# Performance work log

Measured on AMD Instinct MI355X. Metric: run time of the kernel, lower is better.

## Reference

```python
import jax, jax.numpy as jnp
import numpy as np
import math

B, C, T = 8, 512, 4096
CHUNK = 16          # AR_CHUNK_TOK
H = 8               # heads
DH = C // H
CODE_DIM = 96
N_BOOKS = 8
N_EMBED = 1024
EPS = 1e-5
NCH = T // CHUNK


def _posenc(c, t):
    pos = np.arange(t)[:, None].astype(np.float64)
    div = np.exp(np.arange(0, c, 2) * (-math.log(10000.0) / c))
    pe = np.zeros((t, c), np.float32)
    pe[:, 0::2] = np.sin(pos * div)
    pe[:, 1::2] = np.cos(pos * div)
    return jnp.asarray(pe.T)  # [C, t]


def _ln(x, g, b):
    m = x.mean(-1, keepdims=True)
    v = ((x - m) ** 2).mean(-1, keepdims=True)
    return (x - m) * jax.lax.rsqrt(v + EPS) * g + b


def setup_inputs() -> dict:
    ks = jax.random.split(jax.random.key(0), 16)
    w = lambda i, s: jax.random.normal(ks[i], s, jnp.float32) * 0.02
    return dict(
        qa=jax.random.normal(ks[0], (B, C, T), jnp.float32),
        zt=jax.random.normal(ks[1], (B, C, T), jnp.float32),
        lnq_g=jnp.ones((C,), jnp.float32), lnq_b=jnp.zeros((C,), jnp.float32),
        lnkv_g=jnp.ones((C,), jnp.float32), lnkv_b=jnp.zeros((C,), jnp.float32),
        Wq=w(2, (C, C)), Wk=w(3, (C, C)), Wv=w(4, (C, C)), Wo=w(5, (C, C)),
        ffn_g=jnp.ones((C,), jnp.float32), ffn_b=jnp.zeros((C,), jnp.float32),
        W1=w(6, (C, 2 * C)), b1=jnp.zeros((2 * C,), jnp.float32),
        W2=w(7, (2 * C, C)), b2=jnp.zeros((C,), jnp.float32),
        tn_g=jnp.ones((C,), jnp.float32), tn_b=jnp.zeros((C,), jnp.float32),
        scale=jnp.float32(0.08),
        Wd=w(8, (CODE_DIM, C)), bd=jnp.zeros((CODE_DIM,), jnp.float32),
        Wu=w(9, (C, CODE_DIM)), bu=jnp.zeros((C,), jnp.float32),
        books=jax.random.normal(ks[10], (N_BOOKS, N_EMBED, CODE_DIM), jnp.float32) / math.sqrt(CODE_DIM),
    )


def _forward(qa, zt, lnq_g, lnq_b, lnkv_g, lnkv_b, Wq, Wk, Wv, Wo, ffn_g, ffn_b,
             W1, b1, W2, b2, tn_g, tn_b, scale, Wd, bd, Wu, bu, books):
    pe = _posenc(C, CHUNK)  # [C, 16], chunk-local positions as in the torch loop
    qa_c = qa.reshape(B, C, NCH, CHUNK).transpose(2, 0, 1, 3)  # [NCH, B, C, 16]
    zt_c = zt.reshape(B, C, NCH, CHUNK).transpose(2, 0, 1, 3)
    sc = jnp.clip(scale, 0.005, 0.5)

    def split(x):  # [B,16,C] -> [B,H,16,DH]
        return x.reshape(B, CHUNK, H, DH).transpose(0, 2, 1, 3)

    def step(prev_last, xs):
        # zt_prev is [prev chunk's last z_hat token, zeros...]: z_run is zero-initialized
        # and only positions < s are written when chunk s reads it.
        qa_k, zt_k = xs
        zt_prev = jnp.concatenate(
            [prev_last[:, :, None], jnp.zeros((B, C, CHUNK - 1), qa_k.dtype)], axis=-1)
        # CrossPredictor (dropout is identity in eval)
        q = _ln((zt_prev + pe).transpose(0, 2, 1), lnq_g, lnq_b)   # [B,16,C]
        kv = _ln((qa_k + pe).transpose(0, 2, 1), lnkv_g, lnkv_b)   # [B,16,C]
        Q, K, V = split(q @ Wq), split(kv @ Wk), split(kv @ Wv)
        attn = jax.nn.softmax(jnp.einsum('bhqd,bhkd->bhqk', Q, K) / math.sqrt(DH), axis=-1)
        ctx = jnp.einsum('bhqk,bhkd->bhqd', attn, V).transpose(0, 2, 1, 3).reshape(B, CHUNK, C)
        y = ctx @ Wo + q
        y = y + jax.nn.gelu(_ln(y, ffn_g, ffn_b) @ W1 + b1, approximate=False) @ W2 + b2
        z_pred = y.transpose(0, 2, 1)  # [B,C,16]
        # residual -> tanh(TokenNorm) -> scale -> 1x1 conv down
        r = zt_k - jax.lax.stop_gradient(z_pred)
        rN = jnp.tanh(_ln(r.transpose(0, 2, 1), tn_g, tn_b)).transpose(0, 2, 1)
        rD = jnp.einsum('dc,bct->bdt', Wd, sc * rN) + bd[:, None]  # [B,96,16]
        # residual VQ over N_BOOKS codebooks (straight-through)
        x = rD.transpose(0, 2, 1).reshape(B * CHUNK, CODE_DIM)
        residual = x
        q_sum = jnp.zeros_like(x)
        for k in range(N_BOOKS):
            emb = jax.lax.stop_gradient(books[k])
            idx = jnp.argmax(residual @ emb.T - 0.5 * jnp.sum(emb * emb, axis=1), axis=1)
            qv = emb[idx]
            q_sum = q_sum + jax.lax.stop_gradient(qv - residual) + residual
            residual = residual - qv
        qD = q_sum.reshape(B, CHUNK, CODE_DIM).transpose(0, 2, 1)  # [B,96,16]
        z_hat = jnp.einsum('cd,bdt->bct', Wu, qD) + bu[:, None] + z_pred
        return z_hat[:, :, -1], z_hat

    _, ys = jax.lax.scan(step, jnp.zeros((B, C), qa.dtype), (qa_c, zt_c))
    return ys.transpose(1, 2, 0, 3).reshape(B, C, T)  # z_run [B,C,T]


def reference(qa, zt, lnq_g, lnq_b, lnkv_g, lnkv_b, Wq, Wk, Wv, Wo, ffn_g, ffn_b,
              W1, b1, W2, b2, tn_g, tn_b, scale, Wd, bd, Wu, bu, books):
    return _forward(qa, zt, lnq_g, lnq_b, lnkv_g, lnkv_b, Wq, Wk, Wv, Wo, ffn_g, ffn_b,
                    W1, b1, W2, b2, tn_g, tn_b, scale, Wd, bd, Wu, bu, books)
```

## Files before the change

kernel.cpp:

```cpp
#include <hip/hip_runtime.h>
#include <math.h>

#define Bsz 8
#define Cdim 512
#define Tdim 4096
#define NHq 8
#define CD 96
#define NB 8
#define NE 1024
#define NCHq 256
#define Mtok (Bsz*Tdim)
#define M2tok (Bsz*NCHq)

typedef __attribute__((ext_vector_type(8))) short bf16x8;
typedef __attribute__((ext_vector_type(4))) float f32x4;
typedef unsigned int uint;
typedef unsigned short ushort;

__global__ __launch_bounds__(256) void pe_qc_kernel(float* pe_tab, float* qc_ln,
        const float* __restrict__ lnq_g, const float* __restrict__ lnq_b){
  int t = blockIdx.x;
  int tid = threadIdx.x;
  __shared__ float red[256];
  double f = -log(10000.0) / (double)Cdim;
  float v[2];
  #pragma unroll
  for (int u = 0; u < 2; ++u){
    int c = tid + u*256;
    int ce = c & ~1;
    double ang = (double)t * exp(f * (double)ce);
    v[u] = (float)((c & 1) ? cos(ang) : sin(ang));
    pe_tab[t*Cdim + c] = v[u];
  }
  red[tid] = v[0] + v[1]; __syncthreads();
  for (int s = 128; s > 0; s >>= 1){ if (tid < s) red[tid] += red[tid+s]; __syncthreads(); }
  float mean = red[0] * (1.f/512.f); __syncthreads();
  float d0 = v[0]-mean, d1 = v[1]-mean;
  red[tid] = d0*d0 + d1*d1; __syncthreads();
  for (int s = 128; s > 0; s >>= 1){ if (tid < s) red[tid] += red[tid+s]; __syncthreads(); }
  float rstd = 1.0f/sqrtf(red[0]*(1.f/512.f) + 1e-5f);
  qc_ln[t*Cdim + tid]       = d0*rstd*lnq_g[tid]     + lnq_b[tid];
  qc_ln[t*Cdim + tid + 256] = d1*rstd*lnq_g[tid+256] + lnq_b[tid+256];
}

__global__ __launch_bounds__(256) void ln_rows_kernel(const float* __restrict__ src, float* __restrict__ dst,
        const float* __restrict__ g, const float* __restrict__ bia, int mode, const float* __restrict__ scale_ptr){
  int row = blockIdx.x; int tid = threadIdx.x;
  const float* sr = src + (size_t)row*Cdim;
  float v0 = sr[tid], v1 = sr[tid+256];
  __shared__ float red[256];
  red[tid] = v0+v1; __syncthreads();
  for (int s = 128; s > 0; s >>= 1){ if (tid < s) red[tid] += red[tid+s]; __syncthreads(); }
  float mean = red[0]*(1.f/512.f); __syncthreads();
  float d0 = v0-mean, d1 = v1-mean;
  red[tid] = d0*d0 + d1*d1; __syncthreads();
  for (int s = 128; s > 0; s >>= 1){ if (tid < s) red[tid] += red[tid+s]; __syncthreads(); }
  float rstd = 1.0f/sqrtf(red[0]*(1.f/512.f) + 1e-5f);
  float h0 = d0*rstd*g[tid]     + bia[tid];
  float h1 = d1*rstd*g[tid+256] + bia[tid+256];
  if (mode == 1){
    float sc = *scale_ptr; sc = fminf(fmaxf(sc, 0.005f), 0.5f);
    h0 = tanhf(h0)*sc; h1 = tanhf(h1)*sc;
  }
  float* dr = dst + (size_t)row*Cdim;
  dr[tid] = h0; dr[tid+256] = h1;
}

__global__ void tin_kernel(const float* __restrict__ qa, const float* __restrict__ pe_tab, float* __restrict__ rows){
  __shared__ float tile[32][33];
  int b = blockIdx.z, c0 = blockIdx.y*32, t0 = blockIdx.x*32;
  int tx = threadIdx.x, ty = threadIdx.y;
  int t = t0 + tx;
  #pragma unroll
  for (int j = 0; j < 4; j++){
    int c = c0 + ty + j*8;
    tile[ty+j*8][tx] = qa[((size_t)(b*Cdim + c))*Tdim + t] + pe_tab[(t & 15)*Cdim + c];
  }
  __syncthreads();
  #pragma unroll
  for (int j = 0; j < 4; j++){
    int tt = t0 + ty + j*8;
    rows[((size_t)(b*Tdim + tt))*Cdim + c0 + tx] = tile[tx][ty+j*8];
  }
}

__global__ void resid_kernel(const float* __restrict__ zt, const float* __restrict__ zp_rows, float* __restrict__ rows){
  __shared__ float tile[32][33];
  int b = blockIdx.z, c0 = blockIdx.y*32, t0 = blockIdx.x*32;
  int tx = threadIdx.x, ty = threadIdx.y;
  int t = t0 + tx;
  #pragma unroll
  for (int j = 0; j < 4; j++){
    int c = c0 + ty + j*8;
    tile[ty+j*8][tx] = zt[((size_t)(b*Cdim + c))*Tdim + t];
  }
  __syncthreads();
  #pragma unroll
  for (int j = 0; j < 4; j++){
    int tt = t0 + ty + j*8;
    size_t o = ((size_t)(b*Tdim + tt))*Cdim + c0 + tx;
    rows[o] = tile[tx][ty+j*8] - zp_rows[o];
  }
}

__global__ void tout_kernel(const float* __restrict__ rows, float* __restrict__ out){
  __shared__ float tile[32][33];
  int b = blockIdx.z, c0 = blockIdx.y*32, t0 = blockIdx.x*32;
  int tx = threadIdx.x, ty = threadIdx.y;
  #pragma unroll
  for (int j = 0; j < 4; j++){
    int tt = t0 + ty + j*8;
    tile[ty+j*8][tx] = rows[((size_t)(b*Tdim + tt))*Cdim + c0 + tx];
  }
  __syncthreads();
  #pragma unroll
  for (int j = 0; j < 4; j++){
    int c = c0 + ty + j*8;
    out[((size_t)(b*Cdim + c))*Tdim + t0 + tx] = tile[tx][ty+j*8];
  }
}

__global__ void twd_kernel(const float* __restrict__ Wd, float* __restrict__ WdT){
  int i = blockIdx.x*256 + threadIdx.x; if (i >= 96*512) return;
  int kq = i / 96, n = i % 96;
  WdT[i] = Wd[(size_t)n*512 + kq];
}

__global__ void tbt_kernel(const float* __restrict__ books, float* __restrict__ booksT){
  __shared__ float tile[32][33];
  int k = blockIdx.z, d0 = blockIdx.y*32, c0 = blockIdx.x*32;
  int tx = threadIdx.x, ty = threadIdx.y;
  #pragma unroll
  for (int j = 0; j < 4; j++){
    int c = c0 + ty + j*8;
    tile[ty+j*8][tx] = books[((size_t)k*NE + c)*CD + d0 + tx];
  }
  __syncthreads();
  #pragma unroll
  for (int j = 0; j < 4; j++){
    int d = d0 + ty + j*8;
    booksT[(size_t)k*CD*NE + (size_t)d*NE + c0 + tx] = tile[tx][ty+j*8];
  }
}

__global__ void hb_kernel(const float* __restrict__ books, float* __restrict__ hb){
  int j = blockIdx.x*256 + threadIdx.x;
  if (j >= NB*NE) return;
  const float* e = books + (size_t)j*CD;
  float s = 0.f;
  #pragma unroll
  for (int d = 0; d < CD; d++) s = fmaf(e[d], e[d], s);
  hb[j] = 0.5f*s;
}

__device__ __forceinline__ uint pack_hi(float a, float b){
  uint ua = __float_as_uint(a), ub = __float_as_uint(b);
  return (ua >> 16) | (ub & 0xFFFF0000u);
}
__device__ __forceinline__ uint pack_lo(float a, float b){
  float ha = __uint_as_float(__float_as_uint(a) & 0xFFFF0000u);
  float hb = __uint_as_float(__float_as_uint(b) & 0xFFFF0000u);
  return pack_hi(a - ha, b - hb);
}

__global__ void cvtT_kernel(const float* __restrict__ W, ushort* __restrict__ hT, ushort* __restrict__ lT,
        int K, int N){
  __shared__ float tile[32][33];
  int k0 = blockIdx.y*32, n0 = blockIdx.x*32;
  int tx = threadIdx.x, ty = threadIdx.y;
  #pragma unroll
  for (int j = 0; j < 4; j++)
    tile[ty+j*8][tx] = W[(size_t)(k0+ty+j*8)*N + n0+tx];
  __syncthreads();
  #pragma unroll
  for (int j = 0; j < 4; j++){
    int n = n0 + ty + j*8;
    float f = tile[tx][ty+j*8];
    uint u = __float_as_uint(f);
    float hf = __uint_as_float(u & 0xFFFF0000u);
    hT[(size_t)n*K + k0 + tx] = (ushort)(u >> 16);
    lT[(size_t)n*K + k0 + tx] = (ushort)(__float_as_uint(f - hf) >> 16);
  }
}

__global__ void cvtP_kernel(const float* __restrict__ X, ushort* __restrict__ h, ushort* __restrict__ lo, int n){
  int i = blockIdx.x*256 + threadIdx.x; if (i >= n) return;
  float f = X[i];
  uint u = __float_as_uint(f);
  float hf = __uint_as_float(u & 0xFFFF0000u);
  h[i]  = (ushort)(u >> 16);
  lo[i] = (ushort)(__float_as_uint(f - hf) >> 16);
}

__global__ __launch_bounds__(256) void gemm_kernel(const float* __restrict__ A, const float* __restrict__ Bm,
        float* __restrict__ Cm, int M, int N, int K,
        const float* __restrict__ bias, const float* __restrict__ addbuf, int addmode, int act){
  __shared__ float As[16][65];
  __shared__ float Bs[16][64];
  int l = threadIdx.x;
  int tx = l & 15, ty = l >> 4;
  int m0 = blockIdx.y*64, n0 = blockIdx.x*64;
  int ai = l >> 2, ak = (l & 3)*4;
  int bk = l >> 4, bj = (l & 15)*4;
  float acc[4][4] = {{0.f}};
  bool nfull = (n0 + 64 <= N);
  for (int k0 = 0; k0 < K; k0 += 16){
    float4 av = make_float4(0.f, 0.f, 0.f, 0.f);
    if (m0 + ai < M) av = *(const float4*)(A + (size_t)(m0+ai)*K + k0 + ak);
    As[ak][ai] = av.x; As[ak+1][ai] = av.y; As[ak+2][ai] = av.z; As[ak+3][ai] = av.w;
    if (nfull){
      *(float4*)(&Bs[bk][bj]) = *(const float4*)(Bm + (size_t)(k0+bk)*N + n0 + bj);
    } else {
      #pragma unroll
      for (int u = 0; u < 4; u++){
        int n = n0 + bj + u;
        Bs[bk][bj+u] = (n < N) ? Bm[(size_t)(k0+bk)*N + n] : 0.f;
      }
    }
    __syncthreads();
    #pragma unroll
    for (int kk = 0; kk < 16; kk++){
      float a0 = As[kk][ty*4], a1 = As[kk][ty*4+1], a2 = As[kk][ty*4+2], a3 = As[kk][ty*4+3];
      float b0 = Bs[kk][tx*4], b1 = Bs[kk][tx*4+1], b2 = Bs[kk][tx*4+2], b3 = Bs[kk][tx*4+3];
      acc[0][0] = fmaf(a0,b0,acc[0][0]); acc[0][1] = fmaf(a0,b1,acc[0][1]);
      acc[0][2] = fmaf(a0,b2,acc[0][2]); acc[0][3] = fmaf(a0,b3,acc[0][3]);
      acc[1][0] = fmaf(a1,b0,acc[1][0]); acc[1][1] = fmaf(a1,b1,acc[1][1]);
      acc[1][2] = fmaf(a1,b2,acc[1][2]); acc[1][3] = fmaf(a1,b3,acc[1][3]);
      acc[2][0] = fmaf(a2,b0,acc[2][0]); acc[2][1] = fmaf(a2,b1,acc[2][1]);
      acc[2][2] = fmaf(a2,b2,acc[2][2]); acc[2][3] = fmaf(a2,b3,acc[2][3]);
      acc[3][0] = fmaf(a3,b0,acc[3][0]); acc[3][1] = fmaf(a3,b1,acc[3][1]);
      acc[3][2] = fmaf(a3,b2,acc[3][2]); acc[3][3] = fmaf(a3,b3,acc[3][3]);
    }
    __syncthreads();
  }
  #pragma unroll
  for (int r = 0; r < 4; r++){
    int m = m0 + ty*4 + r; if (m >= M) continue;
    #pragma unroll
    for (int c = 0; c < 4; c++){
      int n = n0 + tx*4 + c; if (n >= N) continue;
      float v = acc[r][c];
      if (bias) v += bias[n];
      if (act == 1) v = 0.5f*v*(1.0f + erff(v*0.7071067811865475f));
      if (addmode == 1) v += addbuf[(size_t)(m & 15)*N + n];
      else if (addmode == 2) v += addbuf[(size_t)m*N + n];
      Cm[(size_t)m*N + n] = v;
    }
  }
}

__global__ __launch_bounds__(256, 1) void mgemm_kernel(const float* __restrict__ A,
        const ushort* __restrict__ BhT, const ushort* __restrict__ BlT,
        float* __restrict__ Cm, int M, int N, int K,
        const float* __restrict__ bias, const float* __restrict__ addbuf, int addmode, int act){
  __shared__ __align__(16) ushort Ah[128][32];
  __shared__ __align__(16) ushort Al[128][32];
  __shared__ __align__(16) ushort Bh[128][32];
  __shared__ __align__(16) ushort Bl[128][32];
  int l = threadIdx.x;
  int il = l & 63, wv = l >> 6;
  int wr = wv >> 1, wc = wv & 1;
  int fr = il & 15, fg = il >> 4;
  int m0 = blockIdx.y*128, n0 = blockIdx.x*128;
  int srow = l >> 1, shalf = (l & 1) * 16;
  const float*  Ap  = A   + (size_t)(m0 + srow)*K + shalf;
  const ushort* Bhp = BhT + (size_t)(n0 + srow)*K + shalf;
  const ushort* Blp = BlT + (size_t)(n0 + srow)*K + shalf;
  f32x4 acc[4][4];
  #pragma unroll
  for (int i = 0; i < 4; i++)
    #pragma unroll
    for (int j = 0; j < 4; j++)
      acc[i][j] = (f32x4){0.f, 0.f, 0.f, 0.f};
  for (int k0 = 0; k0 < K; k0 += 32){
    float4 a0 = *(const float4*)(Ap + k0);
    float4 a1 = *(const float4*)(Ap + k0 + 4);
    float4 a2 = *(const float4*)(Ap + k0 + 8);
    float4 a3 = *(const float4*)(Ap + k0 + 12);
    uint4 bh0 = *(const uint4*)(Bhp + k0);
    uint4 bh1 = *(const uint4*)(Bhp + k0 + 8);
    uint4 bl0 = *(const uint4*)(Blp + k0);
    uint4 bl1 = *(const uint4*)(Blp + k0 + 8);
    __syncthreads();
    uint4 h0, h1, l0v, l1v;
    h0.x = pack_hi(a0.x,a0.y); h0.y = pack_hi(a0.z,a0.w);
    h0.z = pack_hi(a1.x,a1.y); h0.w = pack_hi(a1.z,a1.w);
    h1.x = pack_hi(a2.x,a2.y); h1.y = pack_hi(a2.z,a2.w);
    h1.z = pack_hi(a3.x,a3.y); h1.w = pack_hi(a3.z,a3.w);
    l0v.x = pack_lo(a0.x,a0.y); l0v.y = pack_lo(a0.z,a0.w);
    l0v.z = pack_lo(a1.x,a1.y); l0v.w = pack_lo(a1.z,a1.w);
    l1v.x = pack_lo(a2.x,a2.y); l1v.y = pack_lo(a2.z,a2.w);
    l1v.z = pack_lo(a3.x,a3.y); l1v.w = pack_lo(a3.z,a3.w);
    *(uint4*)&Ah[srow][shalf]   = h0;  *(uint4*)&Ah[srow][shalf+8] = h1;
    *(uint4*)&Al[srow][shalf]   = l0v; *(uint4*)&Al[srow][shalf+8] = l1v;
    *(uint4*)&Bh[srow][shalf]   = bh0; *(uint4*)&Bh[srow][shalf+8] = bh1;
    *(uint4*)&Bl[srow][shalf]   = bl0; *(uint4*)&Bl[srow][shalf+8] = bl1;
    __syncthreads();
    bf16x8 afh[4], afl[4], bfh[4], bfl[4];
    #pragma unroll
    for (int q = 0; q < 4; q++){
      afh[q] = *(const bf16x8*)&Ah[wr*64 + q*16 + fr][fg*8];
      afl[q] = *(const bf16x8*)&Al[wr*64 + q*16 + fr][fg*8];
      bfh[q] = *(const bf16x8*)&Bh[wc*64 + q*16 + fr][fg*8];
      bfl[q] = *(const bf16x8*)&Bl[wc*64 + q*16 + fr][fg*8];
    }
    #pragma unroll
    for (int i = 0; i < 4; i++)
      #pragma unroll
      for (int j = 0; j < 4; j++)
        acc[i][j] = __builtin_amdgcn_mfma_f32_16x16x32_bf16(afh[i], bfh[j], acc[i][j], 0, 0, 0);
    #pragma unroll
    for (int i = 0; i < 4; i++)
      #pragma unroll
      for (int j = 0; j < 4; j++)
        acc[i][j] = __builtin_amdgcn_mfma_f32_16x16x32_bf16(afh[i], bfl[j], acc[i][j], 0, 0, 0);
    #pragma unroll
    for (int i = 0; i < 4; i++)
      #pragma unroll
      for (int j = 0; j < 4; j++)
        acc[i][j] = __builtin_amdgcn_mfma_f32_16x16x32_bf16(afl[i], bfh[j], acc[i][j], 0, 0, 0);
  }
  #pragma unroll
  for (int i = 0; i < 4; i++){
    #pragma unroll
    for (int j = 0; j < 4; j++){
      #pragma unroll
      for (int r = 0; r < 4; r++){
        int m = m0 + wr*64 + i*16 + fg*4 + r;
        int n = n0 + wc*64 + j*16 + fr;
        float v = acc[i][j][r];
        if (bias) v += bias[n];
        if (act == 1) v = 0.5f*v*(1.0f + erff(v*0.7071067811865475f));
        if (addmode == 1) v += addbuf[(size_t)(m & 15)*N + n];
        else if (addmode == 2) v += addbuf[(size_t)m*N + n];
        Cm[(size_t)m*N + n] = v;
      }
    }
  }
}

__global__ __launch_bounds__(128) void attn1_kernel(const float* __restrict__ Kb, const float* __restrict__ Vb,
        const float* __restrict__ Qp, float* __restrict__ ctxb){
  int idx = blockIdx.x;
  int b = idx >> 8, ch = idx & 255;
  size_t m0 = (size_t)b*Tdim + ch*16;
  int t = threadIdx.x >> 3, h = threadIdx.x & 7;
  const float* q = Qp + t*Cdim + h*64;
  float qr[64];
  #pragma unroll
  for (int d = 0; d < 64; d += 4){ float4 f = *(const float4*)(q+d); qr[d]=f.x; qr[d+1]=f.y; qr[d+2]=f.z; qr[d+3]=f.w; }
  float s[16];
  #pragma unroll
  for (int k = 0; k < 16; k++){
    const float* kr = Kb + (m0+k)*Cdim + h*64;
    float acc = 0.f;
    #pragma unroll
    for (int d = 0; d < 64; d += 4){
      float4 f = *(const float4*)(kr+d);
      acc = fmaf(qr[d],f.x,acc); acc = fmaf(qr[d+1],f.y,acc);
      acc = fmaf(qr[d+2],f.z,acc); acc = fmaf(qr[d+3],f.w,acc);
    }
    s[k] = acc * 0.125f;
  }
  float mx = s[0];
  #pragma unroll
  for (int k = 1; k < 16; k++) mx = fmaxf(mx, s[k]);
  float sum = 0.f;
  #pragma unroll
  for (int k = 0; k < 16; k++){ s[k] = expf(s[k]-mx); sum += s[k]; }
  float inv = 1.0f/sum;
  float ctx[64];
  #pragma unroll
  for (int d = 0; d < 64; d++) ctx[d] = 0.f;
  #pragma unroll
  for (int k = 0; k < 16; k++){
    float p = s[k]*inv;
    const float* vr = Vb + (m0+k)*Cdim + h*64;
    #pragma unroll
    for (int d = 0; d < 64; d += 4){
      float4 f = *(const float4*)(vr+d);
      ctx[d]=fmaf(p,f.x,ctx[d]); ctx[d+1]=fmaf(p,f.y,ctx[d+1]);
      ctx[d+2]=fmaf(p,f.z,ctx[d+2]); ctx[d+3]=fmaf(p,f.w,ctx[d+3]);
    }
  }
  float* o = ctxb + (m0+t)*Cdim + h*64;
  #pragma unroll
  for (int d = 0; d < 64; d += 4){
    float4 f; f.x=ctx[d]; f.y=ctx[d+1]; f.z=ctx[d+2]; f.w=ctx[d+3];
    *(float4*)(o+d) = f;
  }
}

__global__ __launch_bounds__(64) void attn2_kernel(const float* __restrict__ Kb, const float* __restrict__ Vb,
        const float* __restrict__ Qp, float* __restrict__ ctxb){
  int m2 = blockIdx.x;
  int b = m2 >> 8, ch = m2 & 255;
  size_t m0 = (size_t)b*Tdim + ch*16;
  int h = threadIdx.x;
  if (h >= 8) return;
  const float* q = Qp + (size_t)m2*Cdim + h*64;
  float qr[64];
  #pragma unroll
  for (int d = 0; d < 64; d += 4){ float4 f = *(const float4*)(q+d); qr[d]=f.x; qr[d+1]=f.y; qr[d+2]=f.z; qr[d+3]=f.w; }
  float s[16];
  #pragma unroll
  for (int k = 0; k < 16; k++){
    const float* kr = Kb + (m0+k)*Cdim + h*64;
    float acc = 0.f;
    #pragma unroll
    for (int d = 0; d < 64; d += 4){
      float4 f = *(const float4*)(kr+d);
      acc = fmaf(qr[d],f.x,acc); acc = fmaf(qr[d+1],f.y,acc);
      acc = fmaf(qr[d+2],f.z,acc); acc = fmaf(qr[d+3],f.w,acc);
    }
    s[k] = acc * 0.125f;
  }
  float mx = s[0];
  #pragma unroll
  for (int k = 1; k < 16; k++) mx = fmaxf(mx, s[k]);
  float sum = 0.f;
  #pragma unroll
  for (int k = 0; k < 16; k++){ s[k] = expf(s[k]-mx); sum += s[k]; }
  float inv = 1.0f/sum;
  float ctx[64];
  #pragma unroll
  for (int d = 0; d < 64; d++) ctx[d] = 0.f;
  #pragma unroll
  for (int k = 0; k < 16; k++){
    float p = s[k]*inv;
    const float* vr = Vb + (m0+k)*Cdim + h*64;
    #pragma unroll
    for (int d = 0; d < 64; d += 4){
      float4 f = *(const float4*)(vr+d);
      ctx[d]=fmaf(p,f.x,ctx[d]); ctx[d+1]=fmaf(p,f.y,ctx[d+1]);
      ctx[d+2]=fmaf(p,f.z,ctx[d+2]); ctx[d+3]=fmaf(p,f.w,ctx[d+3]);
    }
  }
  float* o = ctxb + (size_t)m2*Cdim + h*64;
  #pragma unroll
  for (int d = 0; d < 64; d += 4){
    float4 f; f.x=ctx[d]; f.y=ctx[d+1]; f.z=ctx[d+2]; f.w=ctx[d+3];
    *(float4*)(o+d) = f;
  }
}

__global__ __launch_bounds__(256) void q2_kernel(const float* __restrict__ dout, float* __restrict__ p2q,
        const float* __restrict__ g, const float* __restrict__ bia){
  int m2 = blockIdx.x; int tid = threadIdx.x;
  int b = m2 >> 8, ch = m2 & 255;
  int tprev = ch*16 - 1;
  float v0, v1;
  {
    int c = tid;
    float carry = (ch == 0) ? 0.f : dout[((size_t)(b*Cdim + c))*Tdim + tprev];
    v0 = carry + ((c & 1) ? 1.f : 0.f);
  }
  {
    int c = tid + 256;
    float carry = (ch == 0) ? 0.f : dout[((size_t)(b*Cdim + c))*Tdim + tprev];
    v1 = carry + ((c & 1) ? 1.f : 0.f);
  }
  __shared__ float red[256];
  red[tid] = v0+v1; __syncthreads();
  for (int s = 128; s > 0; s >>= 1){ if (tid < s) red[tid] += red[tid+s]; __syncthreads(); }
  float mean = red[0]*(1.f/512.f); __syncthreads();
  float d0 = v0-mean, d1 = v1-mean;
  red[tid] = d0*d0 + d1*d1; __syncthreads();
  for (int s = 128; s > 0; s >>= 1){ if (tid < s) red[tid] += red[tid+s]; __syncthreads(); }
  float rstd = 1.0f/sqrtf(red[0]*(1.f/512.f) + 1e-5f);
  p2q[(size_t)m2*Cdim + tid]       = d0*rstd*g[tid]     + bia[tid];
  p2q[(size_t)m2*Cdim + tid + 256] = d1*rstd*g[tid+256] + bia[tid+256];
}

__global__ __launch_bounds__(256) void r2_kernel(const float* __restrict__ zt, const float* __restrict__ zp,
        float* __restrict__ out){
  int m2 = blockIdx.x; int tid = threadIdx.x;
  int b = m2 >> 8, ch = m2 & 255; int t0 = ch*16;
  #pragma unroll
  for (int u = 0; u < 2; u++){
    int c = tid + u*256;
    out[(size_t)m2*Cdim + c] = zt[((size_t)(b*Cdim + c))*Tdim + t0] - zp[(size_t)m2*Cdim + c];
  }
}

__global__ __launch_bounds__(256) void scatter2_kernel(const float* __restrict__ z, float* __restrict__ dout){
  int m2 = blockIdx.x; int tid = threadIdx.x;
  int b = m2 >> 8, ch = m2 & 255; int t0 = ch*16;
  #pragma unroll
  for (int u = 0; u < 2; u++){
    int c = tid + u*256;
    dout[((size_t)(b*Cdim + c))*Tdim + t0] = z[(size_t)m2*Cdim + c];
  }
}

template<int MT>
__global__ __launch_bounds__(256, 1) void vqg_kernel(float* __restrict__ x,
        const float* __restrict__ books, const float* __restrict__ booksT,
        const float* __restrict__ hb){
  constexpr int MI  = MT/16;
  constexpr int TPT = 256/MT;
  constexpr int F4  = 24/TPT;
  int l = threadIdx.x;
  int tx = l & 15, ty = l >> 4;
  int tok = l / TPT, part = l % TPT;
  size_t tok0 = (size_t)blockIdx.x * MT;
  __shared__ float As[96][MT];
  __shared__ float Es[96][128];
  __shared__ float hs[128];
  __shared__ float sb[MT][16];
  __shared__ int   si[MT][16];
  __shared__ int   sel[MT];
  float* xp = x + (tok0 + tok)*CD;
  #pragma unroll
  for (int j = 0; j < F4; j++){
    int d4 = part*F4 + j;
    float4 v = *(const float4*)(xp + d4*4);
    As[d4*4+0][tok]=v.x; As[d4*4+1][tok]=v.y; As[d4*4+2][tok]=v.z; As[d4*4+3][tok]=v.w;
  }
  for (int k = 0; k < NB; k++){
    const float* bT = booksT + (size_t)k*CD*NE;
    float best[MI]; int bidx[MI];
    #pragma unroll
    for (int i = 0; i < MI; i++){ best[i] = -3.0e38f; bidx[i] = 0; }
    for (int t = 0; t < 8; t++){
      int n0 = t*128;
      __syncthreads();
      #pragma unroll
      for (int j = 0; j < 12; j++){
        int f4 = j*256 + l;
        int d = f4 >> 5, c4 = f4 & 31;
        float4 v = *(const float4*)(bT + (size_t)d*NE + n0 + c4*4);
        *(float4*)(&Es[d][c4*4]) = v;
      }
      if (l < 32){
        float4 hv = *(const float4*)(hb + k*NE + n0 + l*4);
        *(float4*)(&hs[l*4]) = hv;
      }
      __syncthreads();
      float acc[MI][8];
      #pragma unroll
      for (int i = 0; i < MI; i++)
        #pragma unroll
        for (int j = 0; j < 8; j++) acc[i][j] = 0.f;
      #pragma unroll 2
      for (int kk = 0; kk < 96; kk++){
        float av[MI], bw[8];
        #pragma unroll
        for (int g = 0; g < MI/4; g++)
          *(float4*)(av + g*4) = *(const float4*)(&As[kk][g*64 + ty*4]);
        *(float4*)(bw)   = *(const float4*)(&Es[kk][tx*4]);
        *(float4*)(bw+4) = *(const float4*)(&Es[kk][64 + tx*4]);
        #pragma unroll
        for (int i = 0; i < MI; i++)
          #pragma unroll
          for (int j = 0; j < 8; j++)
            acc[i][j] = fmaf(av[i], bw[j], acc[i][j]);
      }
      #pragma unroll
      for (int i = 0; i < MI; i++){
        #pragma unroll
        for (int j = 0; j < 8; j++){
          int cl = (j>>2)*64 + tx*4 + (j&3);
          float s = acc[i][j] - hs[cl];
          if (s > best[i]){ best[i] = s; bidx[i] = n0 + cl; }
        }
      }
    }
    #pragma unroll
    for (int i = 0; i < MI; i++){
      int row = (i>>2)*64 + ty*4 + (i&3);
      sb[row][tx] = best[i]; si[row][tx] = bidx[i];
    }
    __syncthreads();
    if (l < MT){
      float bb = sb[l][0]; int bi = si[l][0];
      #pragma unroll
      for (int t2 = 1; t2 < 16; t2++){
        float b2 = sb[l][t2]; int i2 = si[l][t2];
        if (b2 > bb || (b2 == bb && i2 < bi)){ bb = b2; bi = i2; }
      }
      sel[l] = bi;
    }
    __syncthreads();
    int s = sel[tok];
    const float* e = books + ((size_t)k*NE + s)*CD;
    #pragma unroll
    for (int j = 0; j < F4; j++){
      int d4 = part*F4 + j;
      float4 v = *(const float4*)(e + d4*4);
      As[d4*4+0][tok] -= v.x; As[d4*4+1][tok] -= v.y;
      As[d4*4+2][tok] -= v.z; As[d4*4+3][tok] -= v.w;
    }
  }
  #pragma unroll
  for (int j = 0; j < F4; j++){
    int d4 = part*F4 + j;
    float4 xo = *(const float4*)(xp + d4*4);
    float4 q;
    q.x = xo.x - As[d4*4+0][tok];
    q.y = xo.y - As[d4*4+1][tok];
    q.z = xo.z - As[d4*4+2][tok];
    q.w = xo.w - As[d4*4+3][tok];
    *(float4*)(xp + d4*4) = q;
  }
}

extern "C" void kernel_launch(void* const* d_in, const int* in_sizes, int n_in,
                              void* d_out, int out_size, void* d_ws, size_t ws_size,
                              hipStream_t stream) {
  const float* qa    = (const float*)d_in[0];
  const float* zt    = (const float*)d_in[1];
  const float* lnq_g = (const float*)d_in[2];
  const float* lnq_b = (const float*)d_in[3];
  const float* lnkv_g= (const float*)d_in[4];
  const float* lnkv_b= (const float*)d_in[5];
  const float* Wq    = (const float*)d_in[6];
  const float* Wk    = (const float*)d_in[7];
  const float* Wv    = (const float*)d_in[8];
  const float* Wo    = (const float*)d_in[9];
  const float* ffn_g = (const float*)d_in[10];
  const float* ffn_b = (const float*)d_in[11];
  const float* W1    = (const float*)d_in[12];
  const float* b1    = (const float*)d_in[13];
  const float* W2    = (const float*)d_in[14];
  const float* b2    = (const float*)d_in[15];
  const float* tn_g  = (const float*)d_in[16];
  const float* tn_b  = (const float*)d_in[17];
  const float* scale = (const float*)d_in[18];
  const float* Wd    = (const float*)d_in[19];
  const float* bd    = (const float*)d_in[20];
  const float* Wu    = (const float*)d_in[21];
  const float* bu    = (const float*)d_in[22];
  const float* books = (const float*)d_in[23];
  float* out = (float*)d_out;

  float* ws = (float*)d_ws;
  size_t off = 0;
  float* pe_tab  = ws + off; off += 16*512;
  float* qc_ln   = ws + off; off += 16*512;
  float* qc_proj = ws + off; off += 16*512;
  float* WdT     = ws + off; off += 512*96;
  float* hbuf    = ws + off; off += 8*1024;
  ushort* wub = (ushort*)(ws + off); off += 2146304;
  ushort* WqTh = wub;            ushort* WqTl = WqTh + 262144;
  ushort* WkTh = WqTl + 262144;  ushort* WkTl = WkTh + 262144;
  ushort* WvTh = WkTl + 262144;  ushort* WvTl = WvTh + 262144;
  ushort* WoTh = WvTl + 262144;  ushort* WoTl = WoTh + 262144;
  ushort* W1Th = WoTl + 262144;  ushort* W1Tl = W1Th + 524288;
  ushort* W2Th = W1Tl + 524288;  ushort* W2Tl = W2Th + 524288;
  ushort* WuPh = W2Tl + 524288;  ushort* WuPl = WuPh + 49152;
  float* bA      = ws + off; off += (size_t)Mtok*512;
  float* bK      = ws + off; off += (size_t)Mtok*512;
  float* bV      = ws + off; off += (size_t)Mtok*512;
  float* bH      = ws + off; off += (size_t)4096*1024;
  float* bX      = bH;
  float* booksTp = bH + (size_t)Mtok*CD;
  float* bY      = out;

  float* p2q   = bA;
  float* p2Qp  = bA + 1048576;
  float* p2ctx = bA + 2*1048576;
  float* p2y   = bA + 3*1048576;
  float* p2lny = bA + 4*1048576;
  float* p2h   = bA + 5*1048576;
  float* p2r   = bA + 7*1048576;
  float* p2x   = bA + 8*1048576;
  float* p2z   = bA + 8*1048576 + 196608;

  dim3 tpb32(32, 8);
  dim3 tgrid(Tdim/32, Cdim/32, Bsz);

  hipLaunchKernelGGL(pe_qc_kernel, dim3(16), dim3(256), 0, stream, pe_tab, qc_ln, lnq_g, lnq_b);
  hipLaunchKernelGGL(twd_kernel, dim3((96*512+255)/256), dim3(256), 0, stream, Wd, WdT);
  hipLaunchKernelGGL(hb_kernel, dim3((NB*NE+255)/256), dim3(256), 0, stream, books, hbuf);
  hipLaunchKernelGGL(cvtT_kernel, dim3(16, 16), tpb32, 0, stream, Wq, WqTh, WqTl, 512, 512);
  hipLaunchKernelGGL(cvtT_kernel, dim3(16, 16), tpb32, 0, stream, Wk, WkTh, WkTl, 512, 512);
  hipLaunchKernelGGL(cvtT_kernel, dim3(16, 16), tpb32, 0, stream, Wv, WvTh, WvTl, 512, 512);
  hipLaunchKernelGGL(cvtT_kernel, dim3(16, 16), tpb32, 0, stream, Wo, WoTh, WoTl, 512, 512);
  hipLaunchKernelGGL(cvtT_kernel, dim3(32, 16), tpb32, 0, stream, W1, W1Th, W1Tl, 512, 1024);
  hipLaunchKernelGGL(cvtT_kernel, dim3(16, 32), tpb32, 0, stream, W2, W2Th, W2Tl, 1024, 512);
  hipLaunchKernelGGL(cvtP_kernel, dim3((512*96+255)/256), dim3(256), 0, stream, Wu, WuPh, WuPl, 512*96);

  hipLaunchKernelGGL(tin_kernel, tgrid, tpb32, 0, stream, qa, pe_tab, bA);
  hipLaunchKernelGGL(ln_rows_kernel, dim3(Mtok), dim3(256), 0, stream, bA, bA, lnkv_g, lnkv_b, 0, scale);
  hipLaunchKernelGGL(mgemm_kernel, dim3(4, Mtok/128), dim3(256), 0, stream, bA, WkTh, WkTl, bK, Mtok, 512, 512,
                     (const float*)nullptr, (const float*)nullptr, 0, 0);
  hipLaunchKernelGGL(mgemm_kernel, dim3(4, Mtok/128), dim3(256), 0, stream, bA, WvTh, WvTl, bV, Mtok, 512, 512,
                     (const float*)nullptr, (const float*)nullptr, 0, 0);
  hipLaunchKernelGGL(gemm_kernel, dim3(8, 1), dim3(256), 0, stream, qc_ln, Wq, qc_proj, 16, 512, 512,
                     (const float*)nullptr, (const float*)nullptr, 0, 0);

  hipLaunchKernelGGL(attn1_kernel, dim3(M2tok), dim3(128), 0, stream, bK, bV, qc_proj, bA);
  hipLaunchKernelGGL(mgemm_kernel, dim3(4, Mtok/128), dim3(256), 0, stream, bA, WoTh, WoTl, bY, Mtok, 512, 512,
                     (const float*)nullptr, qc_ln, 1, 0);
  hipLaunchKernelGGL(ln_rows_kernel, dim3(Mtok), dim3(256), 0, stream, bY, bA, ffn_g, ffn_b, 0, scale);
  for (int p = 0; p < 8; p++){
    size_t mo = (size_t)p*4096;
    hipLaunchKernelGGL(mgemm_kernel, dim3(8, 4096/128), dim3(256), 0, stream, bA + mo*512, W1Th, W1Tl, bH, 4096, 1024, 512,
                       b1, (const float*)nullptr, 0, 1);
    hipLaunchKernelGGL(mgemm_kernel, dim3(4, 4096/128), dim3(256), 0, stream, bH, W2Th, W2Tl, bY + mo*512, 4096, 512, 1024,
                       b2, bY + mo*512, 2, 0);
  }

  hipLaunchKernelGGL(resid_kernel, tgrid, tpb32, 0, stream, zt, bY, bA);
  hipLaunchKernelGGL(ln_rows_kernel, dim3(Mtok), dim3(256), 0, stream, bA, bA, tn_g, tn_b, 1, scale);
  hipLaunchKernelGGL(gemm_kernel, dim3(2, Mtok/64), dim3(256), 0, stream, bA, WdT, bX, Mtok, 96, 512,
                     bd, (const float*)nullptr, 0, 0);
  hipLaunchKernelGGL(tbt_kernel, dim3(NE/32, CD/32, NB), tpb32, 0, stream, books, booksTp);
  hipLaunchKernelGGL(vqg_kernel<128>, dim3(Mtok/128), dim3(256), 0, stream, bX, books, booksTp, hbuf);
  hipLaunchKernelGGL(mgemm_kernel, dim3(4, Mtok/128), dim3(256), 0, stream, bX, WuPh, WuPl, bA, Mtok, 512, 96,
                     bu, bY, 2, 0);
  hipLaunchKernelGGL(tout_kernel, tgrid, tpb32, 0, stream, bA, out);

  hipLaunchKernelGGL(q2_kernel, dim3(M2tok), dim3(256), 0, stream, out, p2q, lnq_g, lnq_b);
  hipLaunchKernelGGL(mgemm_kernel, dim3(4, M2tok/128), dim3(256), 0, stream, p2q, WqTh, WqTl, p2Qp, M2tok, 512, 512,
                     (const float*)nullptr, (const float*)nullptr, 0, 0);
  hipLaunchKernelGGL(attn2_kernel, dim3(M2tok), dim3(64), 0, stream, bK, bV, p2Qp, p2ctx);
  hipLaunchKernelGGL(mgemm_kernel, dim3(4, M2tok/128), dim3(256), 0, stream, p2ctx, WoTh, WoTl, p2y, M2tok, 512, 512,
                     (const float*)nullptr, p2q, 2, 0);
  hipLaunchKernelGGL(ln_rows_kernel, dim3(M2tok), dim3(256), 0, stream, p2y, p2lny, ffn_g, ffn_b, 0, scale);
  hipLaunchKernelGGL(mgemm_kernel, dim3(8, M2tok/128), dim3(256), 0, stream, p2lny, W1Th, W1Tl, p2h, M2tok, 1024, 512,
                     b1, (const float*)nullptr, 0, 1);
  hipLaunchKernelGGL(mgemm_kernel, dim3(4, M2tok/128), dim3(256), 0, stream, p2h, W2Th, W2Tl, p2y, M2tok, 512, 1024,
                     b2, p2y, 2, 0);
  hipLaunchKernelGGL(r2_kernel, dim3(M2tok), dim3(256), 0, stream, zt, p2y, p2r);
  hipLaunchKernelGGL(ln_rows_kernel, dim3(M2tok), dim3(256), 0, stream, p2r, p2r, tn_g, tn_b, 1, scale);
  hipLaunchKernelGGL(gemm_kernel, dim3(2, M2tok/64), dim3(256), 0, stream, p2r, WdT, p2x, M2tok, 96, 512,
                     bd, (const float*)nullptr, 0, 0);
  hipLaunchKernelGGL(vqg_kernel<64>, dim3(M2tok/64), dim3(256), 0, stream, p2x, books, booksTp, hbuf);
  hipLaunchKernelGGL(mgemm_kernel, dim3(4, M2tok/128), dim3(256), 0, stream, p2x, WuPh, WuPl, p2z, M2tok, 512, 96,
                     bu, p2y, 2, 0);
  hipLaunchKernelGGL(scatter2_kernel, dim3(M2tok), dim3(256), 0, stream, p2z, out);

  (void)in_sizes; (void)n_in; (void)out_size; (void)ws_size;
}
```

Baseline: 3.733 ms.

## Widen VQ codebook tile and split small-batch VQ across codebook chunks

The large-batch VQ kernel now uses a 128x256 register tile (8x16 per thread) with 256-code chunks and a shuffle-based argmax instead of a shared-memory reduction. The small second-pass VQ, which only had 32 blocks, is split into per-codebook launches: one kernel computes partial argmaxes over 8 code chunks in parallel, and a second merges them and updates the residual. This aims to raise arithmetic intensity in the big pass and to fill the GPU in the small pass. The cost is more registers and LDS in vq1, and 16 extra launches plus workspace round-trips in the second pass.

```diff
diff --git a/kernel.cpp b/kernel.cpp
--- a/kernel.cpp
+++ b/kernel.cpp
@@ -493,73 +493,68 @@
   }
 }
 
-template<int MT>
-__global__ __launch_bounds__(256, 1) void vqg_kernel(float* __restrict__ x,
+__global__ __launch_bounds__(256, 1) void vq1_kernel(float* __restrict__ x,
         const float* __restrict__ books, const float* __restrict__ booksT,
         const float* __restrict__ hb){
-  constexpr int MI  = MT/16;
-  constexpr int TPT = 256/MT;
-  constexpr int F4  = 24/TPT;
   int l = threadIdx.x;
   int tx = l & 15, ty = l >> 4;
-  int tok = l / TPT, part = l % TPT;
-  size_t tok0 = (size_t)blockIdx.x * MT;
-  __shared__ float As[96][MT];
-  __shared__ float Es[96][128];
-  __shared__ float hs[128];
-  __shared__ float sb[MT][16];
-  __shared__ int   si[MT][16];
-  __shared__ int   sel[MT];
+  int tok = l >> 1, part = l & 1;
+  size_t tok0 = (size_t)blockIdx.x * 128;
+  __shared__ float As[96][128];
+  __shared__ float Es[96][256];
+  __shared__ float hs[256];
+  __shared__ int   sel[128];
   float* xp = x + (tok0 + tok)*CD;
   #pragma unroll
-  for (int j = 0; j < F4; j++){
-    int d4 = part*F4 + j;
+  for (int j = 0; j < 12; j++){
+    int d4 = part*12 + j;
     float4 v = *(const float4*)(xp + d4*4);
     As[d4*4+0][tok]=v.x; As[d4*4+1][tok]=v.y; As[d4*4+2][tok]=v.z; As[d4*4+3][tok]=v.w;
   }
   for (int k = 0; k < NB; k++){
     const float* bT = booksT + (size_t)k*CD*NE;
-    float best[MI]; int bidx[MI];
-    #pragma unroll
-    for (int i = 0; i < MI; i++){ best[i] = -3.0e38f; bidx[i] = 0; }
-    for (int t = 0; t < 8; t++){
-      int n0 = t*128;
+    const float* hk = hb + k*NE;
+    float best[8]; int bidx[8];
+    #pragma unroll
+    for (int i = 0; i < 8; i++){ best[i] = -3.0e38f; bidx[i] = 0; }
+    for (int t = 0; t < 4; t++){
+      int n0 = t*256;
       __syncthreads();
       #pragma unroll
-      for (int j = 0; j < 12; j++){
+      for (int j = 0; j < 24; j++){
         int f4 = j*256 + l;
-        int d = f4 >> 5, c4 = f4 & 31;
+        int d = f4 >> 6, c4 = f4 & 63;
         float4 v = *(const float4*)(bT + (size_t)d*NE + n0 + c4*4);
         *(float4*)(&Es[d][c4*4]) = v;
       }
-      if (l < 32){
-        float4 hv = *(const float4*)(hb + k*NE + n0 + l*4);
+      if (l < 64){
+        float4 hv = *(const float4*)(hk + n0 + l*4);
         *(float4*)(&hs[l*4]) = hv;
       }
       __syncthreads();
-      float acc[MI][8];
-      #pragma unroll
-      for (int i = 0; i < MI; i++)
+      float acc[8][16];
+      #pragma unroll
+      for (int i = 0; i < 8; i++)
         #pragma unroll
-        for (int j = 0; j < 8; j++) acc[i][j] = 0.f;
+        for (int j = 0; j < 16; j++) acc[i][j] = 0.f;
       #pragma unroll 2
       for (int kk = 0; kk < 96; kk++){
-        float av[MI], bw[8];
+        float av[8], bw[16];
+        *(float4*)(av)   = *(const float4*)(&As[kk][ty*8]);
+        *(float4*)(av+4) = *(const float4*)(&As[kk][ty*8+4]);
         #pragma unroll
-        for (int g = 0; g < MI/4; g++)
-          *(float4*)(av + g*4) = *(const float4*)(&As[kk][g*64 + ty*4]);
-        *(float4*)(bw)   = *(const float4*)(&Es[kk][tx*4]);
-        *(float4*)(bw+4) = *(const float4*)(&Es[kk][64 + tx*4]);
+        for (int p = 0; p < 4; p++)
+          *(float4*)(bw + p*4) = *(const float4*)(&Es[kk][p*64 + tx*4]);
         #pragma unroll
-        for (int i = 0; i < MI; i++)
+        for (int i = 0; i < 8; i++)
           #pragma unroll
-          for (int j = 0; j < 8; j++)
+          for (int j = 0; j < 16; j++)
             acc[i][j] = fmaf(av[i], bw[j], acc[i][j]);
       }
       #pragma unroll
-      for (int i = 0; i < MI; i++){
+      for (int i = 0; i < 8; i++){
         #pragma unroll
-        for (int j = 0; j < 8; j++){
+        for (int j = 0; j < 16; j++){
           int cl = (j>>2)*64 + tx*4 + (j&3);
           float s = acc[i][j] - hs[cl];
           if (s > best[i]){ best[i] = s; bidx[i] = n0 + cl; }
@@ -567,34 +562,30 @@
       }
     }
     #pragma unroll
-    for (int i = 0; i < MI; i++){
-      int row = (i>>2)*64 + ty*4 + (i&3);
-      sb[row][tx] = best[i]; si[row][tx] = bidx[i];
-    }
-    __syncthreads();
-    if (l < MT){
-      float bb = sb[l][0]; int bi = si[l][0];
-      #pragma unroll
-      for (int t2 = 1; t2 < 16; t2++){
-        float b2 = sb[l][t2]; int i2 = si[l][t2];
-        if (b2 > bb || (b2 == bb && i2 < bi)){ bb = b2; bi = i2; }
+    for (int i = 0; i < 8; i++){
+      float s = best[i]; int idx = bidx[i];
+      #pragma unroll
+      for (int m = 1; m < 16; m <<= 1){
+        float os = __shfl_xor(s, m);
+        int   oi = __shfl_xor(idx, m);
+        if (os > s || (os == s && oi < idx)){ s = os; idx = oi; }
       }
-      sel[l] = bi;
+      if (tx == 0) sel[ty*8 + i] = idx;
     }
     __syncthreads();
     int s = sel[tok];
     const float* e = books + ((size_t)k*NE + s)*CD;
     #pragma unroll
-    for (int j = 0; j < F4; j++){
-      int d4 = part*F4 + j;
+    for (int j = 0; j < 12; j++){
+      int d4 = part*12 + j;
       float4 v = *(const float4*)(e + d4*4);
       As[d4*4+0][tok] -= v.x; As[d4*4+1][tok] -= v.y;
       As[d4*4+2][tok] -= v.z; As[d4*4+3][tok] -= v.w;
     }
   }
   #pragma unroll
-  for (int j = 0; j < F4; j++){
-    int d4 = part*F4 + j;
+  for (int j = 0; j < 12; j++){
+    int d4 = part*12 + j;
     float4 xo = *(const float4*)(xp + d4*4);
     float4 q;
     q.x = xo.x - As[d4*4+0][tok];
@@ -602,6 +593,118 @@
     q.z = xo.z - As[d4*4+2][tok];
     q.w = xo.w - As[d4*4+3][tok];
     *(float4*)(xp + d4*4) = q;
+  }
+}
+
+__global__ __launch_bounds__(256, 2) void vq2a_kernel(const float* __restrict__ src,
+        const float* __restrict__ booksT, const float* __restrict__ hb,
+        float* __restrict__ ps, int* __restrict__ pi, int k){
+  int l = threadIdx.x;
+  int tx = l & 15, ty = l >> 4;
+  int cb = blockIdx.x;
+  int tok0 = blockIdx.y * 64;
+  int n0 = cb * 128;
+  __shared__ float As[96][64];
+  __shared__ float Es[96][128];
+  __shared__ float hs[128];
+  {
+    int tok = l >> 2, part = l & 3;
+    const float* sp = src + (size_t)(tok0 + tok)*CD;
+    #pragma unroll
+    for (int j = 0; j < 6; j++){
+      int d4 = part*6 + j;
+      float4 v = *(const float4*)(sp + d4*4);
+      As[d4*4+0][tok]=v.x; As[d4*4+1][tok]=v.y; As[d4*4+2][tok]=v.z; As[d4*4+3][tok]=v.w;
+    }
+  }
+  const float* bT = booksT + (size_t)k*CD*NE;
+  #pragma unroll
+  for (int j = 0; j < 12; j++){
+    int f4 = j*256 + l;
+    int d = f4 >> 5, c4 = f4 & 31;
+    float4 v = *(const float4*)(bT + (size_t)d*NE + n0 + c4*4);
+    *(float4*)(&Es[d][c4*4]) = v;
+  }
+  if (l < 32){
+    float4 hv = *(const float4*)(hb + k*NE + n0 + l*4);
+    *(float4*)(&hs[l*4]) = hv;
+  }
+  __syncthreads();
+  float acc[4][8];
+  #pragma unroll
+  for (int i = 0; i < 4; i++)
+    #pragma unroll
+    for (int j = 0; j < 8; j++) acc[i][j] = 0.f;
+  #pragma unroll 2
+  for (int kk = 0; kk < 96; kk++){
+    float av[4], bw[8];
+    *(float4*)(av)   = *(const float4*)(&As[kk][ty*4]);
+    *(float4*)(bw)   = *(const float4*)(&Es[kk][tx*4]);
+    *(float4*)(bw+4) = *(const float4*)(&Es[kk][64 + tx*4]);
+    #pragma unroll
+    for (int i = 0; i < 4; i++)
+      #pragma unroll
+      for (int j = 0; j < 8; j++)
+        acc[i][j] = fmaf(av[i], bw[j], acc[i][j]);
+  }
+  #pragma unroll
+  for (int i = 0; i < 4; i++){
+    float best = -3.0e38f; int bidx = 0;
+    #pragma unroll
+    for (int j = 0; j < 8; j++){
+      int cl = (j>>2)*64 + tx*4 + (j&3);
+      float s = acc[i][j] - hs[cl];
+      if (s > best){ best = s; bidx = n0 + cl; }
+    }
+    #pragma unroll
+    for (int m = 1; m < 16; m <<= 1){
+      float os = __shfl_xor(best, m);
+      int   oi = __shfl_xor(bidx, m);
+      if (os > best || (os == best && oi < bidx)){ best = os; bidx = oi; }
+    }
+    if (tx == 0){
+      int row = tok0 + ty*4 + i;
+      ps[cb*M2tok + row] = best;
+      pi[cb*M2tok + row] = bidx;
+    }
+  }
+}
+
+__global__ __launch_bounds__(256) void vq2b_kernel(float* __restrict__ x, float* __restrict__ res,
+        const float* __restrict__ books, const float* __restrict__ ps, const int* __restrict__ pi, int k){
+  int l = threadIdx.x;
+  int tok = blockIdx.x*32 + (l >> 3);
+  int part = l & 7;
+  float bb = ps[tok]; int bi = pi[tok];
+  #pragma unroll
+  for (int c = 1; c < 8; c++){
+    float s2 = ps[c*M2tok + tok]; int i2 = pi[c*M2tok + tok];
+    if (s2 > bb || (s2 == bb && i2 < bi)){ bb = s2; bi = i2; }
+  }
+  const float* e = books + ((size_t)k*NE + bi)*CD + part*12;
+  const float* sp = ((k == 0) ? (const float*)x : (const float*)res) + (size_t)tok*CD + part*12;
+  float r[12];
+  #pragma unroll
+  for (int j = 0; j < 12; j += 4){
+    float4 sv = *(const float4*)(sp + j);
+    float4 ev = *(const float4*)(e + j);
+    r[j]=sv.x-ev.x; r[j+1]=sv.y-ev.y; r[j+2]=sv.z-ev.z; r[j+3]=sv.w-ev.w;
+  }
+  if (k < NB-1){
+    float* rp = res + (size_t)tok*CD + part*12;
+    #pragma unroll
+    for (int j = 0; j < 12; j += 4){
+      float4 v; v.x=r[j]; v.y=r[j+1]; v.z=r[j+2]; v.w=r[j+3];
+      *(float4*)(rp + j) = v;
+    }
+  } else {
+    float* xq = x + (size_t)tok*CD + part*12;
+    #pragma unroll
+    for (int j = 0; j < 12; j += 4){
+      float4 xo = *(const float4*)(xq + j);
+      float4 v; v.x=xo.x-r[j]; v.y=xo.y-r[j+1]; v.z=xo.z-r[j+2]; v.w=xo.w-r[j+3];
+      *(float4*)(xq + j) = v;
+    }
   }
 }
 
@@ -666,6 +769,9 @@
   float* p2r   = bA + 7*1048576;
   float* p2x   = bA + 8*1048576;
   float* p2z   = bA + 8*1048576 + 196608;
+  float* res2  = bA + 10*1048576;
+  float* ps2   = bA + 10*1048576 + 196608;
+  int*   pi2   = (int*)(bA + 10*1048576 + 196608 + 16384);
 
   dim3 tpb32(32, 8);
   dim3 tgrid(Tdim/32, Cdim/32, Bsz);
@@ -707,7 +813,7 @@
   hipLaunchKernelGGL(gemm_kernel, dim3(2, Mtok/64), dim3(256), 0, stream, bA, WdT, bX, Mtok, 96, 512,
                      bd, (const float*)nullptr, 0, 0);
   hipLaunchKernelGGL(tbt_kernel, dim3(NE/32, CD/32, NB), tpb32, 0, stream, books, booksTp);
-  hipLaunchKernelGGL(vqg_kernel<128>, dim3(Mtok/128), dim3(256), 0, stream, bX, books, booksTp, hbuf);
+  hipLaunchKernelGGL(vq1_kernel, dim3(Mtok/128), dim3(256), 0, stream, bX, books, booksTp, hbuf);
   hipLaunchKernelGGL(mgemm_kernel, dim3(4, Mtok/128), dim3(256), 0, stream, bX, WuPh, WuPl, bA, Mtok, 512, 96,
                      bu, bY, 2, 0);
   hipLaunchKernelGGL(tout_kernel, tgrid, tpb32, 0, stream, bA, out);
@@ -727,7 +833,12 @@
   hipLaunchKernelGGL(ln_rows_kernel, dim3(M2tok), dim3(256), 0, stream, p2r, p2r, tn_g, tn_b, 1, scale);
   hipLaunchKernelGGL(gemm_kernel, dim3(2, M2tok/64), dim3(256), 0, stream, p2r, WdT, p2x, M2tok, 96, 512,
                      bd, (const float*)nullptr, 0, 0);
-  hipLaunchKernelGGL(vqg_kernel<64>, dim3(M2tok/64), dim3(256), 0, stream, p2x, books, booksTp, hbuf);
+  for (int k = 0; k < NB; k++){
+    hipLaunchKernelGGL(vq2a_kernel, dim3(8, M2tok/64), dim3(256), 0, stream,
+                       (k == 0 ? p2x : res2), booksTp, hbuf, ps2, pi2, k);
+    hipLaunchKernelGGL(vq2b_kernel, dim3(M2tok/32), dim3(256), 0, stream,
+                       p2x, res2, books, ps2, pi2, k);
+  }
   hipLaunchKernelGGL(mgemm_kernel, dim3(4, M2tok/128), dim3(256), 0, stream, p2x, WuPh, WuPl, p2z, M2tok, 512, 96,
                      bu, p2y, 2, 0);
   hipLaunchKernelGGL(scatter2_kernel, dim3(M2tok), dim3(256), 0, stream, p2z, out);
```

Result: faster. 3.335 ms (-10.7%).
